# Performance work log

Measured on AMD Instinct MI355X. Metric: run time of the kernel, lower is better.

The kernel has to match this reference:

```python
import jax, jax.numpy as jnp
import numpy as np

B, C, H, W = 4, 768, 64, 64
NC_PRED = 200   # classes in preds/text (!= 171 to trigger retrieval path)
NC_MEM = 171    # memory/text_coco classes
TC = 256        # transform_channels
OC = 768        # out_channels
BN_EPS = 1e-5


def setup_inputs() -> dict:
    key = jax.random.key(0)
    ks = jax.random.split(key, 32)
    n = lambda k, s, sc=1.0: jax.random.normal(k, s, jnp.float32) * sc
    g = lambda k, c: 1.0 + 0.1 * jax.random.normal(k, (c,), jnp.float32)
    inp = {
        'feats': n(ks[0], (B, C, H, W)),
        'preds': n(ks[1], (B, NC_PRED, H, W)),
        'text': n(ks[2], (1, NC_PRED, 1, C)),
        'memory': n(ks[3], (NC_MEM, 1, C)),      # self.memory buffer
        'text_mem': n(ks[4], (NC_MEM, 1, C)),    # self.text buffer
        # query_project: two 1x1 conv + BN + ReLU
        'qw1': n(ks[5], (TC, C), C ** -0.5), 'qg1': g(ks[6], TC), 'qb1': n(ks[7], (TC,), 0.1),
        'qw2': n(ks[8], (TC, TC), TC ** -0.5), 'qg2': g(ks[9], TC), 'qb2': n(ks[10], (TC,), 0.1),
        # key_project: two 1x1 conv + BN + ReLU
        'kw1': n(ks[11], (TC, C), C ** -0.5), 'kg1': g(ks[12], TC), 'kb1': n(ks[13], (TC,), 0.1),
        'kw2': n(ks[14], (TC, TC), TC ** -0.5), 'kg2': g(ks[15], TC), 'kb2': n(ks[16], (TC,), 0.1),
        # value_project: 1x1 conv + BN + ReLU
        'vw': n(ks[17], (TC, C), C ** -0.5), 'vg': g(ks[18], TC), 'vb': n(ks[19], (TC,), 0.1),
        # out_project: 1x1 conv + BN + ReLU (TC -> C)
        'ow': n(ks[20], (C, TC), TC ** -0.5), 'og': g(ks[21], C), 'ob': n(ks[22], (C,), 0.1),
        # bottleneck: 3x3 conv (2C -> OC) + BN + ReLU
        'bw': n(ks[23], (OC, 2 * C, 3, 3), (2 * C * 9) ** -0.5), 'bg': g(ks[24], OC), 'bb': n(ks[25], (OC,), 0.1),
    }
    return inp


def _cbr(x, w, gamma, beta):
    # 1x1 conv (no bias) + eval-mode BN (mean=0, var=1) + ReLU
    y = jnp.einsum('oc,bchw->bohw', w, x)
    s = (gamma / jnp.sqrt(1.0 + BN_EPS))[None, :, None, None]
    return jax.nn.relu(y * s + beta[None, :, None, None])


def _forward(feats, preds, text, memory, text_mem,
             qw1, qg1, qb1, qw2, qg2, qb2,
             kw1, kg1, kb1, kw2, kg2, kb2,
             vw, vg, vb, ow, og, ob, bw, bg, bb):
    b, c, h, w = feats.shape
    nc = preds.shape[1]
    # softmax class weights per pixel: [B*H*W, NC]
    wcls = jax.nn.softmax(preds.transpose(0, 2, 3, 1).reshape(-1, nc), axis=-1)
    # --- retrieval: cosine sim + argmax + gather (nc != 171 branch) ---
    t = text[0, :, 0, :]          # [NC_PRED, C]
    tc = text_mem[:, 0, :]        # [NC_MEM, C]
    mem = memory[:, 0, :]         # [NC_MEM, C]
    den = jnp.linalg.norm(t, axis=1)[:, None] * jnp.linalg.norm(tc, axis=1)[None, :]
    sim = (t @ tc.T) / jnp.maximum(den, 1e-8)
    idx = jnp.argmax(sim, axis=1)            # [NC_PRED]
    D = mem[idx]                             # gathered memory rows [NC_PRED, C]
    # soft aggregation
    sel = (wcls @ D).reshape(b, h, w, c).transpose(0, 3, 1, 2)  # [B,C,H,W]
    # --- self-attention: query=feats, key/value=selected memory ---
    q = _cbr(_cbr(feats, qw1, qg1, qb1), qw2, qg2, qb2).reshape(b, TC, h * w).transpose(0, 2, 1)  # [B,HW,TC]
    k = _cbr(_cbr(sel, kw1, kg1, kb1), kw2, kg2, kb2).reshape(b, TC, h * w)                        # [B,TC,HW]
    v = _cbr(sel, vw, vg, vb).reshape(b, TC, h * w).transpose(0, 2, 1)                             # [B,HW,TC]
    att = jax.nn.softmax(jnp.einsum('bqc,bck->bqk', q, k) * (TC ** -0.5), axis=-1)                 # [B,HW,HW]
    ctx = jnp.einsum('bqk,bkc->bqc', att, v).transpose(0, 2, 1).reshape(b, TC, h, w)
    sel_out = _cbr(ctx, ow, og, ob)          # [B,C,H,W]
    # --- bottleneck: 3x3 conv + BN + ReLU on concat ---
    x = jnp.concatenate([feats, sel_out], axis=1)
    y = jax.lax.conv_general_dilated(x, bw, (1, 1), 'SAME',
                                     dimension_numbers=('NCHW', 'OIHW', 'NCHW'))
    s = (bg / jnp.sqrt(1.0 + BN_EPS))[None, :, None, None]
    return jax.nn.relu(y * s + bb[None, :, None, None])


def reference(feats, preds, text, memory, text_mem,
              qw1, qg1, qb1, qw2, qg2, qb2,
              kw1, kg1, kb1, kw2, kg2, kb2,
              vw, vg, vb, ow, og, ob, bw, bg, bb):
    return _forward(feats, preds, text, memory, text_mem,
                    qw1, qg1, qb1, qw2, qg2, qb2,
                    kw1, kg1, kb1, kw2, kg2, kb2,
                    vw, vg, vb, ow, og, ob, bw, bg, bb)
```

## Files before the change

kernel.cpp:

```cpp
#include <hip/hip_runtime.h>
#include <stdint.h>

typedef unsigned short u16;
typedef __attribute__((ext_vector_type(8))) short short8;
typedef __attribute__((ext_vector_type(4))) float f32x4;

#define RSQC 0.9999950000374997f
#define OUT_ELEMS 12582912

__device__ __forceinline__ float bf2f(u16 u) {
  union { uint32_t i; float f; } v; v.i = ((uint32_t)u) << 16; return v.f;
}
__device__ __forceinline__ u16 f2bf(float f) {
  union { uint32_t i; float f; } v; v.f = f;
  uint32_t i = v.i;
  i += 0x7fffu + ((i >> 16) & 1u);
  return (u16)(i >> 16);
}

__global__ __launch_bounds__(256) void probe_fill(float* out, float val) {
  for (size_t i = (size_t)blockIdx.x * 256 + threadIdx.x; i < OUT_ELEMS; i += (size_t)gridDim.x * 256)
    out[i] = val;
}


__global__ __launch_bounds__(64) void sim_argmax(const float* __restrict__ text,
                                                 const float* __restrict__ tmem,
                                                 int* __restrict__ idx) {
  const int i = blockIdx.x, lane = threadIdx.x;
  const float* t = text + (size_t)i * 768;
  float nt = 0.f;
  for (int c = lane; c < 768; c += 64) { float x = t[c]; nt += x * x; }
#pragma unroll
  for (int m = 32; m; m >>= 1) nt += __shfl_xor(nt, m);
  nt = sqrtf(nt);
  float best = -1e30f; int bj = 0x7fffffff;
  for (int j = lane; j < 171; j += 64) {
    const float* tc = tmem + (size_t)j * 768;
    float dot = 0.f, nc = 0.f;
    for (int c = 0; c < 768; ++c) {
      float y = tc[c];
      dot += t[c] * y;
      nc += y * y;
    }
    float den = fmaxf(nt * sqrtf(nc), 1e-8f);
    float s = dot / den;
    if (s > best || (s == best && j < bj)) { best = s; bj = j; }
  }
#pragma unroll
  for (int m = 32; m; m >>= 1) {
    float ob = __shfl_xor(best, m); int oj = __shfl_xor(bj, m);
    if (ob > best || (ob == best && oj < bj)) { best = ob; bj = oj; }
  }
  if (lane == 0) idx[i] = bj;
}

__global__ __launch_bounds__(256) void build_d(const float* __restrict__ memory,
                                               const int* __restrict__ idx,
                                               u16* __restrict__ D) {
  int i = blockIdx.x * 256 + threadIdx.x;
  if (i >= 256 * 768) return;
  int c = i % 768, j = i / 768;
  u16 v = 0;
  if (j < 200) {
    int ii = idx[j];
    ii = ii < 0 ? 0 : (ii > 170 ? 170 : ii);
    v = f2bf(memory[(size_t)ii * 768 + c]);
  }
  D[i] = v;
}

__global__ __launch_bounds__(256) void wcls_kernel(const float* __restrict__ preds,
                                                   u16* __restrict__ wcls) {
  __shared__ float red[4][64];
  const int tid = threadIdx.x;
  const int p = tid & 63, q = tid >> 6;
  const int pos = blockIdx.x * 64 + p;
  const int b = pos >> 12, hw = pos & 4095;
  const float* pp = preds + (size_t)b * 200 * 4096 + hw;
  const int nlo = q * 50, nhi = nlo + 50;
  float mx = -1e30f;
  for (int n = nlo; n < nhi; ++n) mx = fmaxf(mx, pp[(size_t)n * 4096]);
  red[q][p] = mx;
  __syncthreads();
  const float m = fmaxf(fmaxf(red[0][p], red[1][p]), fmaxf(red[2][p], red[3][p]));
  __syncthreads();
  float s = 0.f;
  for (int n = nlo; n < nhi; ++n) s += __expf(pp[(size_t)n * 4096] - m);
  red[q][p] = s;
  __syncthreads();
  const float inv = 1.f / (red[0][p] + red[1][p] + red[2][p] + red[3][p]);
  u16* w = wcls + (size_t)pos * 256;
#pragma unroll
  for (int c8 = 0; c8 < 8; ++c8) {
    short8 v;
    const int base = q * 64 + c8 * 8;
#pragma unroll
    for (int j = 0; j < 8; ++j) {
      const int n = base + j;
      float e = (n < 200) ? __expf(pp[(size_t)n * 4096] - m) * inv : 0.f;
      v[j] = (short)f2bf(e);
    }
    *(short8*)&w[base] = v;
  }
}

__global__ __launch_bounds__(256) void transpose_feats(const float* __restrict__ feats,
                                                       u16* __restrict__ ft) {
  __shared__ u16 t[64][65];
  const int bz = blockIdx.z, c0 = blockIdx.y * 64, p0 = blockIdx.x * 64;
  const int col = threadIdx.x & 63, row4 = threadIdx.x >> 6;
  const float* src = feats + ((size_t)bz * 768 + c0) * 4096 + p0;
#pragma unroll
  for (int i = 0; i < 16; ++i) {
    int ci = i * 4 + row4;
    t[ci][col] = f2bf(src[(size_t)ci * 4096 + col]);
  }
  __syncthreads();
  u16* dst = ft + ((size_t)bz * 4096 + p0) * 768 + c0;
#pragma unroll
  for (int i = 0; i < 16; ++i) {
    int pi = i * 4 + row4;
    dst[(size_t)pi * 768 + col] = t[col][pi];
  }
}

__global__ __launch_bounds__(256) void cast_all(
    const float* __restrict__ s0, u16* __restrict__ d0,
    const float* __restrict__ s1, u16* __restrict__ d1,
    const float* __restrict__ s2, u16* __restrict__ d2,
    const float* __restrict__ s3, u16* __restrict__ d3,
    const float* __restrict__ s4, u16* __restrict__ d4,
    const float* __restrict__ s5, u16* __restrict__ d5) {
  int i = blockIdx.x * 256 + threadIdx.x;
  if (i < 196608) d0[i] = f2bf(s0[i]);
  else if (i < 393216) d1[i - 196608] = f2bf(s1[i - 196608]);
  else if (i < 589824) d2[i - 393216] = f2bf(s2[i - 393216]);
  else if (i < 786432) d3[i - 589824] = f2bf(s3[i - 589824]);
  else if (i < 851968) d4[i - 786432] = f2bf(s4[i - 786432]);
  else if (i < 917504) d5[i - 851968] = f2bf(s5[i - 851968]);
}

__global__ __launch_bounds__(256) void repack_frag(const float* __restrict__ bw,
                                                   u16* __restrict__ w9f, int c_base) {
  size_t i = (size_t)blockIdx.x * 256 + threadIdx.x;
  if (i >= (size_t)5308416) return;
  int j = (int)(i & 7);
  int lane = (int)((i >> 3) & 63);
  int rem = (int)(i >> 9);
  int mfrag = rem % 48;
  int pt = rem / 48;
  int tap = pt % 9;
  int kc = pt / 9;
  int o = mfrag * 16 + (lane & 15);
  int c = kc * 32 + (lane >> 4) * 8 + j;
  w9f[i] = f2bf(bw[((size_t)o * 1536 + c_base + c) * 9 + tap]);
}


template <bool EP>
__global__ __launch_bounds__(256) void gemm_std(
    const u16* __restrict__ A, const u16* __restrict__ Bt, u16* __restrict__ out,
    const float* __restrict__ g, const float* __restrict__ bia,
    int N, int K, int lda, int ldb) {
  __shared__ __attribute__((aligned(16))) u16 As[2][128 * 32];
  __shared__ __attribute__((aligned(16))) u16 Bs[2][128 * 32];
  const int tid = threadIdx.x, lane = tid & 63, wv = tid >> 6;
  const int wr = wv >> 1, wc = wv & 1;
  const int m0 = blockIdx.y * 128, n0 = blockIdx.x * 128;
  const int r0 = lane >> 2, ksl = (lane & 3) * 8;
  const int wofs = (lane >> 2) * 32 + (((lane & 3) ^ ((lane >> 3) & 3)) << 3);
  const int rsl = (((lane >> 4) ^ ((lane >> 1) & 3)) << 3);
  f32x4 acc[4][4] = {};
  const int nt = K >> 5;

  short8 a0[2], b0[2], a1[2], b1[2];
  auto LOAD = [&](int t, short8 av[2], short8 bv[2]) {
    const int k0 = t << 5;
#pragma unroll
    for (int i = 0; i < 2; ++i) {
      const int row = (wv * 2 + i) * 16 + r0;
      av[i] = *(const short8*)(A + (size_t)(m0 + row) * lda + k0 + ksl);
      bv[i] = *(const short8*)(Bt + (size_t)(n0 + row) * ldb + k0 + ksl);
    }
  };
  auto STORE = [&](int buf, short8 av[2], short8 bv[2]) {
#pragma unroll
    for (int i = 0; i < 2; ++i) {
      const int o = (wv * 2 + i) * 512 + wofs;
      *(short8*)&As[buf][o] = av[i];
      *(short8*)&Bs[buf][o] = bv[i];
    }
  };
  auto COMPUTE = [&](int buf) {
    short8 a[4], b[4];
#pragma unroll
    for (int mi = 0; mi < 4; ++mi)
      a[mi] = *(const short8*)&As[buf][(wr * 4 + mi) * 512 + (lane & 15) * 32 + rsl];
#pragma unroll
    for (int ni = 0; ni < 4; ++ni)
      b[ni] = *(const short8*)&Bs[buf][(wc * 4 + ni) * 512 + (lane & 15) * 32 + rsl];
#pragma unroll
    for (int mi = 0; mi < 4; ++mi)
#pragma unroll
      for (int ni = 0; ni < 4; ++ni)
        acc[mi][ni] = __builtin_amdgcn_mfma_f32_16x16x32_bf16(a[mi], b[ni], acc[mi][ni], 0, 0, 0);
  };

  LOAD(0, a0, b0);
  for (int t = 0; t < nt; t += 2) {
    STORE(0, a0, b0);
    __syncthreads();
    LOAD(t + 1, a1, b1);
    COMPUTE(0);
    STORE(1, a1, b1);
    __syncthreads();
    if (t + 2 < nt) LOAD(t + 2, a0, b0);
    COMPUTE(1);
  }
  const int mb = m0 + wr * 64 + ((lane >> 4) << 2);
  const int nb = n0 + wc * 64 + (lane & 15);
#pragma unroll
  for (int ni = 0; ni < 4; ++ni) {
    const int n = nb + ni * 16;
    float s = 1.f, bb_ = 0.f;
    if (EP) { s = g[n] * RSQC; bb_ = bia[n]; }
#pragma unroll
    for (int mi = 0; mi < 4; ++mi)
#pragma unroll
      for (int r = 0; r < 4; ++r) {
        float v = acc[mi][ni][r];
        if (EP) v = fmaxf(v * s + bb_, 0.f);
        out[(size_t)(mb + mi * 16 + r) * N + n] = f2bf(v);
      }
  }
}

__global__ __launch_bounds__(256) void gemm_swv(
    const u16* __restrict__ A, const u16* __restrict__ Bt, u16* __restrict__ out,
    const float* __restrict__ g, const float* __restrict__ bia,
    int Mtot, int K, int lda, int ldb) {
  __shared__ __attribute__((aligned(16))) u16 As[2][128 * 32];
  __shared__ __attribute__((aligned(16))) u16 Bs[2][128 * 32];
  const int tid = threadIdx.x, lane = tid & 63, wv = tid >> 6;
  const int wr = wv >> 1, wc = wv & 1;
  const int m0 = blockIdx.y * 128, n0 = blockIdx.x * 128;
  const int r0 = lane >> 2, ksl = (lane & 3) * 8;
  const int wofs = (lane >> 2) * 32 + (((lane & 3) ^ ((lane >> 3) & 3)) << 3);
  const int rsl = (((lane >> 4) ^ ((lane >> 1) & 3)) << 3);
  f32x4 acc[4][4] = {};
  const int nt = K >> 5;

  short8 a0[2], b0[2], a1[2], b1[2];
  auto LOAD = [&](int t, short8 av[2], short8 bv[2]) {
    const int k0 = t << 5;
#pragma unroll
    for (int i = 0; i < 2; ++i) {
      const int row = (wv * 2 + i) * 16 + r0;
      av[i] = *(const short8*)(A + (size_t)(m0 + row) * lda + k0 + ksl);
      bv[i] = *(const short8*)(Bt + (size_t)(n0 + row) * ldb + k0 + ksl);
    }
  };
  auto STORE = [&](int buf, short8 av[2], short8 bv[2]) {
#pragma unroll
    for (int i = 0; i < 2; ++i) {
      const int o = (wv * 2 + i) * 512 + wofs;
      *(short8*)&As[buf][o] = av[i];
      *(short8*)&Bs[buf][o] = bv[i];
    }
  };
  auto COMPUTE = [&](int buf) {
    short8 a[4], b[4];
#pragma unroll
    for (int mi = 0; mi < 4; ++mi)
      a[mi] = *(const short8*)&As[buf][(wr * 4 + mi) * 512 + (lane & 15) * 32 + rsl];
#pragma unroll
    for (int ni = 0; ni < 4; ++ni)
      b[ni] = *(const short8*)&Bs[buf][(wc * 4 + ni) * 512 + (lane & 15) * 32 + rsl];
#pragma unroll
    for (int mi = 0; mi < 4; ++mi)
#pragma unroll
      for (int ni = 0; ni < 4; ++ni)
        acc[mi][ni] = __builtin_amdgcn_mfma_f32_16x16x32_bf16(a[mi], b[ni], acc[mi][ni], 0, 0, 0);
  };

  LOAD(0, a0, b0);
  for (int t = 0; t < nt; t += 2) {
    STORE(0, a0, b0);
    __syncthreads();
    LOAD(t + 1, a1, b1);
    COMPUTE(0);
    STORE(1, a1, b1);
    __syncthreads();
    if (t + 2 < nt) LOAD(t + 2, a0, b0);
    COMPUTE(1);
  }
  const int mb = m0 + wr * 64 + ((lane >> 4) << 2);
  const int nb = n0 + wc * 64 + (lane & 15);
#pragma unroll
  for (int mi = 0; mi < 4; ++mi)
#pragma unroll
    for (int r = 0; r < 4; ++r) {
      const int m = mb + mi * 16 + r;
      const float s = g[m] * RSQC, bb_ = bia[m];
#pragma unroll
      for (int ni = 0; ni < 4; ++ni) {
        const int n = nb + ni * 16;
        out[((size_t)(n >> 12) * Mtot + m) * 4096 + (n & 4095)] =
            f2bf(fmaxf(acc[mi][ni][r] * s + bb_, 0.f));
      }
    }
}

template <int MODE>
__global__ __launch_bounds__(256) void conv_frag(
    const u16* __restrict__ Af, const u16* __restrict__ X, float* out,
    const float* __restrict__ g, const float* __restrict__ bia) {
  __shared__ __attribute__((aligned(16))) u16 Hb[2][264 * 32];
  const int tid = threadIdx.x, lane = tid & 63, wv = tid >> 6;
  const int wr = wv >> 1, wc = wv & 1;
  const int id = blockIdx.y * 128 + blockIdx.x;
  const int xcd = id & 7, sl = id >> 3;
  const int m0 = (sl % 6) * 128;
  const int n0 = (xcd * 16 + sl / 6) * 128;
  f32x4 acc[4][4] = {};

  int vmask[4];
#pragma unroll
  for (int i = 0; i < 4; ++i) {
    const int hw = (n0 + wc * 64 + i * 16 + (lane & 15)) & 4095;
    const int h = hw >> 6, w = hw & 63;
    int m = 0;
#pragma unroll
    for (int t = 0; t < 9; ++t)
      if ((unsigned)(h + t / 3 - 1) < 64u && (unsigned)(w + t % 3 - 1) < 64u) m |= 1 << t;
    vmask[i] = m;
  }

  const int fb = (m0 >> 4) + wr * 4;
  auto aload = [&](int kc, int tap, short8 d[4]) {
    const u16* base = Af + ((size_t)((kc * 9 + tap) * 48 + fb) << 9) + lane * 8;
#pragma unroll
    for (int mi = 0; mi < 4; ++mi) d[mi] = *(const short8*)(base + (mi << 9));
  };
  auto hload = [&](int kc, short8 hreg[5]) {
#pragma unroll
    for (int j = 0; j < 5; ++j) {
      const int cid = tid + j * 256;
      if (cid < 1032) {
        int q = n0 - 65 + (cid >> 2);
        q = q < 0 ? 0 : (q > 16383 ? 16383 : q);
        hreg[j] = *(const short8*)(X + (size_t)q * 768 + kc * 32 + (cid & 3) * 8);
      }
    }
  };
  auto hwrite = [&](int buf, short8 hreg[5]) {
#pragma unroll
    for (int j = 0; j < 5; ++j) {
      const int cid = tid + j * 256;
      if (cid < 1032) {
        const int s = cid & 3, row = cid >> 2;
        *(short8*)((char*)&Hb[buf][0] + row * 64 + ((s ^ ((row >> 1) & 3)) << 4)) = hreg[j];
      }
    }
  };

  short8 hreg[5];
  hload(0, hreg);
  hwrite(0, hreg);
  __syncthreads();

  short8 acur[4], anxt[4];
  aload(0, 0, acur);
  int p = 0;
  for (int kc = 0; kc < 24; ++kc) {
    if (kc < 23) hload(kc + 1, hreg);
#pragma unroll
    for (int tap = 0; tap < 9; ++tap) {
      const int nk = (tap == 8) ? (kc == 23 ? 23 : kc + 1) : kc;
      const int ntp = (tap == 8) ? 0 : tap + 1;
      aload(nk, ntp, anxt);
      const int shift = (tap / 3 - 1) * 64 + (tap % 3 - 1);
#pragma unroll
      for (int ni = 0; ni < 4; ++ni) {
        const int hrow = wc * 64 + ni * 16 + (lane & 15) + 65 + shift;
        short8 bv = *(const short8*)((const char*)&Hb[p][0] + hrow * 64 +
                                     (((lane >> 4) ^ ((hrow >> 1) & 3)) << 4));
        short8 z = {};
        if (!((vmask[ni] >> tap) & 1)) bv = z;
#pragma unroll
        for (int mi = 0; mi < 4; ++mi)
          acc[mi][ni] = __builtin_amdgcn_mfma_f32_16x16x32_bf16(acur[mi], bv, acc[mi][ni], 0, 0, 0);
      }
#pragma unroll
      for (int mi = 0; mi < 4; ++mi) acur[mi] = anxt[mi];
    }
    if (kc < 23) {
      hwrite(p ^ 1, hreg);
      __syncthreads();
      p ^= 1;
    }
  }
  const int mb = m0 + wr * 64 + ((lane >> 4) << 2);
  const int nb = n0 + wc * 64 + (lane & 15);
#pragma unroll
  for (int mi = 0; mi < 4; ++mi)
#pragma unroll
    for (int r = 0; r < 4; ++r) {
      const int m = mb + mi * 16 + r;
      float s = 0.f, bb_ = 0.f;
      if (MODE == 2) { s = g[m] * RSQC; bb_ = bia[m]; }
#pragma unroll
      for (int ni = 0; ni < 4; ++ni) {
        const int n = nb + ni * 16;
        const size_t oidx = ((size_t)(n >> 12) * 768 + m) * 4096 + (n & 4095);
        if (MODE == 1) out[oidx] = acc[mi][ni][r];
        else out[oidx] = fmaxf((acc[mi][ni][r] + out[oidx]) * s + bb_, 0.f);
      }
    }
}

__global__ __launch_bounds__(256) void flash_attn(const u16* Q,
                                                  const u16* __restrict__ Kg,
                                                  const u16* __restrict__ Vt,
                                                  u16* ctx) {
  __shared__ __attribute__((aligned(16))) u16 KVs[64 * 256];
  __shared__ __attribute__((aligned(16))) u16 Ps[4096];
  const int tid = threadIdx.x, lane = tid & 63, wv = tid >> 6;
  const int b = blockIdx.y, q0 = blockIdx.x * 64;
  const u16* qb = Q + ((size_t)b * 4096 + q0) * 256;
  const u16* kb = Kg + (size_t)b * 4096 * 256;
  const u16* vb = Vt + (size_t)b * 256 * 4096;
  const float scale = 0.0625f;

  short8 qf[8];
  {
    const int arow = wv * 16 + (lane & 15);
    const u16* qrow = qb + (size_t)arow * 256 + (lane >> 4) * 8;
#pragma unroll
    for (int kk = 0; kk < 8; ++kk) qf[kk] = *(const short8*)(qrow + kk * 32);
  }
  float mreg[4] = {-1e30f, -1e30f, -1e30f, -1e30f};
  float lsum[4] = {0.f, 0.f, 0.f, 0.f};
  f32x4 o[16] = {};

  for (int t = 0; t < 64; ++t) {
    {
      const int r = tid >> 5, sb = (tid & 31) * 16;
      const char* ksrc = (const char*)(kb + (size_t)t * 64 * 256);
#pragma unroll
      for (int i = 0; i < 8; ++i) {
        int row = i * 8 + r;
        short8 v = *(const short8*)(ksrc + (size_t)row * 512 + sb);
        *(short8*)((char*)KVs + row * 512 + (sb ^ ((row & 7) << 4))) = v;
      }
    }
    __syncthreads();
    f32x4 s4[4] = {};
    __builtin_amdgcn_s_setprio(1);
#pragma unroll
    for (int kk = 0; kk < 8; ++kk) {
      const int cb = (kk * 32 + ((lane >> 4) * 8)) * 2;
#pragma unroll
      for (int ni = 0; ni < 4; ++ni) {
        const int brow = ni * 16 + (lane & 15);
        short8 bb = *(const short8*)((const char*)KVs + brow * 512 + (cb ^ ((brow & 7) << 4)));
        s4[ni] = __builtin_amdgcn_mfma_f32_16x16x32_bf16(qf[kk], bb, s4[ni], 0, 0, 0);
      }
    }
    __builtin_amdgcn_s_setprio(0);
    float al[4], p[4][4];
#pragma unroll
    for (int r = 0; r < 4; ++r) {
      float v0 = fmaxf(fmaxf(s4[0][r], s4[1][r]), fmaxf(s4[2][r], s4[3][r]));
      v0 = fmaxf(v0, __shfl_xor(v0, 1));
      v0 = fmaxf(v0, __shfl_xor(v0, 2));
      v0 = fmaxf(v0, __shfl_xor(v0, 4));
      v0 = fmaxf(v0, __shfl_xor(v0, 8));
      const float mn = fmaxf(mreg[r], v0 * scale);
      al[r] = __expf(mreg[r] - mn);
      mreg[r] = mn;
      float srow = 0.f;
#pragma unroll
      for (int ni = 0; ni < 4; ++ni) {
        float pv = __expf(s4[ni][r] * scale - mn);
        p[ni][r] = pv;
        srow += pv;
      }
      srow += __shfl_xor(srow, 1);
      srow += __shfl_xor(srow, 2);
      srow += __shfl_xor(srow, 4);
      srow += __shfl_xor(srow, 8);
      lsum[r] = lsum[r] * al[r] + srow;
    }
#pragma unroll
    for (int nf = 0; nf < 16; ++nf)
#pragma unroll
      for (int r = 0; r < 4; ++r) o[nf][r] *= al[r];
    {
      char* pbase = (char*)Ps + wv * 2048;
#pragma unroll
      for (int ni = 0; ni < 4; ++ni)
#pragma unroll
        for (int r = 0; r < 4; ++r) {
          const int row = ((lane >> 4) << 2) + r, col = ni * 16 + (lane & 15);
          *(u16*)(pbase + row * 128 + ((col * 2) ^ ((row & 7) << 4))) = f2bf(p[ni][r]);
        }
    }
    __syncthreads();
    {
      const int slot = tid & 7;
#pragma unroll
      for (int i = 0; i < 8; ++i) {
        const int cc = i * 32 + (tid >> 3);
        short8 v = *(const short8*)((const char*)vb + ((size_t)cc * 4096 + t * 64) * 2 + slot * 16);
        *(short8*)((char*)KVs + cc * 128 + ((slot * 16) ^ ((cc & 7) << 4))) = v;
      }
    }
    __syncthreads();
    short8 pa[2];
#pragma unroll
    for (int kk = 0; kk < 2; ++kk) {
      const int row = lane & 15;
      const int cb = (kk * 32 + ((lane >> 4) * 8)) * 2;
      pa[kk] = *(const short8*)((const char*)Ps + wv * 2048 + row * 128 + (cb ^ ((row & 7) << 4)));
    }
    __builtin_amdgcn_s_setprio(1);
#pragma unroll
    for (int nf = 0; nf < 16; ++nf) {
      const int crow = nf * 16 + (lane & 15);
#pragma unroll
      for (int kk = 0; kk < 2; ++kk) {
        const int kb2 = (kk * 32 + ((lane >> 4) * 8)) * 2;
        short8 bb = *(const short8*)((const char*)KVs + crow * 128 + (kb2 ^ ((crow & 7) << 4)));
        o[nf] = __builtin_amdgcn_mfma_f32_16x16x32_bf16(pa[kk], bb, o[nf], 0, 0, 0);
      }
    }
    __builtin_amdgcn_s_setprio(0);
    __syncthreads();
  }
  u16* cb_ = ctx + ((size_t)b * 4096 + q0) * 256;
#pragma unroll
  for (int r = 0; r < 4; ++r) {
    const int row = wv * 16 + ((lane >> 4) << 2) + r;
    const float inv = 1.f / lsum[r];
#pragma unroll
    for (int nf = 0; nf < 16; ++nf) {
      const int col = nf * 16 + (lane & 15);
      cb_[(size_t)row * 256 + col] = f2bf(o[nf][r] * inv);
    }
  }
}


extern "C" void kernel_launch(void* const* d_in, const int* in_sizes, int n_in,
                              void* d_out, int out_size, void* d_ws, size_t ws_size,
                              hipStream_t stream) {
  (void)in_sizes; (void)n_in; (void)out_size;
  const float* feats  = (const float*)d_in[0];
  const float* preds  = (const float*)d_in[1];
  const float* text   = (const float*)d_in[2];
  const float* memory = (const float*)d_in[3];
  const float* tmem   = (const float*)d_in[4];
  const float* qw1 = (const float*)d_in[5];  const float* qg1 = (const float*)d_in[6];  const float* qb1 = (const float*)d_in[7];
  const float* qw2 = (const float*)d_in[8];  const float* qg2 = (const float*)d_in[9];  const float* qb2 = (const float*)d_in[10];
  const float* kw1 = (const float*)d_in[11]; const float* kg1 = (const float*)d_in[12]; const float* kb1 = (const float*)d_in[13];
  const float* kw2 = (const float*)d_in[14]; const float* kg2 = (const float*)d_in[15]; const float* kb2 = (const float*)d_in[16];
  const float* vw  = (const float*)d_in[17]; const float* vg  = (const float*)d_in[18]; const float* vb  = (const float*)d_in[19];
  const float* ow  = (const float*)d_in[20]; const float* og  = (const float*)d_in[21]; const float* ob  = (const float*)d_in[22];
  const float* bw  = (const float*)d_in[23]; const float* bg  = (const float*)d_in[24]; const float* bb  = (const float*)d_in[25];

  float* dout = (float*)d_out;
  char* ws = (char*)d_ws;
  u16* featsT = (u16*)(ws);
  u16* selout = (u16*)(ws + 25165824);
  u16* S2     = (u16*)(ws + 50331648);
  u16* qw1c   = (u16*)(ws + 58720256);
  u16* kw1c   = (u16*)(ws + 59113472);
  u16* vwc    = (u16*)(ws + 59506688);
  u16* owc    = (u16*)(ws + 59899904);
  u16* qw2c   = (u16*)(ws + 60293120);
  u16* kw2c   = (u16*)(ws + 60424192);
  u16* w9     = S2;
  const size_t WS_NEED = 60948480;
  u16* D   = selout;
  u16* KD  = (u16*)((char*)selout + 393216);
  u16* VD  = (u16*)((char*)selout + 524288);
  int* idx = (int*)((char*)selout + 655360);
  u16* O0 = (u16*)dout;
  u16* O1 = O0 + 4194304;
  u16* O2 = O0 + 8388608;

  if (ws_size < WS_NEED) {
    probe_fill<<<2048, 256, 0, stream>>>(dout, 1000.0f);
    return;
  }

  u16* wcls = O0;
  u16* k1 = S2, *q1 = S2;
  u16* kbuf = O1, *vT = O2;
  u16* qbuf = O0, *ctx = O0;

  sim_argmax<<<200, 64, 0, stream>>>(text, tmem, idx);
  build_d<<<768, 256, 0, stream>>>(memory, idx, D);
  wcls_kernel<<<256, 256, 0, stream>>>(preds, wcls);
  transpose_feats<<<dim3(64, 12, 4), 256, 0, stream>>>(feats, featsT);
  cast_all<<<3584, 256, 0, stream>>>(qw1, qw1c, kw1, kw1c, vw, vwc, ow, owc, qw2, qw2c, kw2, kw2c);

  gemm_std<false><<<dim3(2, 2), 256, 0, stream>>>(kw1c, D, KD, nullptr, nullptr, 256, 768, 768, 768);
  gemm_std<false><<<dim3(2, 2), 256, 0, stream>>>(vwc, D, VD, nullptr, nullptr, 256, 768, 768, 768);

  gemm_std<true><<<dim3(2, 128), 256, 0, stream>>>(wcls, KD, k1, kg1, kb1, 256, 256, 256, 256);
  gemm_std<true><<<dim3(2, 128), 256, 0, stream>>>(k1, kw2c, kbuf, kg2, kb2, 256, 256, 256, 256);
  gemm_swv<<<dim3(128, 2), 256, 0, stream>>>(VD, wcls, vT, vg, vb, 256, 256, 256, 256);
  gemm_std<true><<<dim3(2, 128), 256, 0, stream>>>(featsT, qw1c, q1, qg1, qb1, 256, 768, 768, 768);
  gemm_std<true><<<dim3(2, 128), 256, 0, stream>>>(q1, qw2c, qbuf, qg2, qb2, 256, 256, 256, 256);
  flash_attn<<<dim3(64, 4), 256, 0, stream>>>(qbuf, kbuf, vT, ctx);
  gemm_std<true><<<dim3(6, 128), 256, 0, stream>>>(ctx, owc, selout, og, ob, 768, 256, 256, 256);
  repack_frag<<<20736, 256, 0, stream>>>(bw, w9, 0);
  conv_frag<1><<<dim3(128, 6), 256, 0, stream>>>(w9, featsT, dout, nullptr, nullptr);
  repack_frag<<<20736, 256, 0, stream>>>(bw, w9, 768);
  conv_frag<2><<<dim3(128, 6), 256, 0, stream>>>(w9, selout, dout, bg, bb);
}
```

Baseline: 815.4 us.

## Vectorize weight repack and stage conv halo via direct global-to-LDS loads

```diff
diff --git a/kernel.cpp b/kernel.cpp
--- a/kernel.cpp
+++ b/kernel.cpp
@@ -16,6 +16,11 @@
   uint32_t i = v.i;
   i += 0x7fffu + ((i >> 16) & 1u);
   return (u16)(i >> 16);
+}
+__device__ __forceinline__ void gload16(const u16* g, u16* l) {
+  __builtin_amdgcn_global_load_lds(
+      (const __attribute__((address_space(1))) uint32_t*)g,
+      (__attribute__((address_space(3))) uint32_t*)l, 16, 0, 0);
 }
 
 __global__ __launch_bounds__(256) void probe_fill(float* out, float val) {
@@ -141,22 +146,25 @@
   else if (i < 917504) d5[i - 851968] = f2bf(s5[i - 851968]);
 }
 
-__global__ __launch_bounds__(256) void repack_frag(const float* __restrict__ bw,
-                                                   u16* __restrict__ w9f, int c_base) {
-  size_t i = (size_t)blockIdx.x * 256 + threadIdx.x;
-  if (i >= (size_t)5308416) return;
-  int j = (int)(i & 7);
-  int lane = (int)((i >> 3) & 63);
-  int rem = (int)(i >> 9);
-  int mfrag = rem % 48;
-  int pt = rem / 48;
-  int tap = pt % 9;
-  int kc = pt / 9;
-  int o = mfrag * 16 + (lane & 15);
-  int c = kc * 32 + (lane >> 4) * 8 + j;
-  w9f[i] = f2bf(bw[((size_t)o * 1536 + c_base + c) * 9 + tap]);
-}
-
+__global__ __launch_bounds__(256) void repack2(const float* __restrict__ bw,
+                                               u16* __restrict__ w9f, int c_base) {
+  const int gid = blockIdx.x * 4 + (threadIdx.x >> 6);
+  const int lane = threadIdx.x & 63;
+  const int mfrag = gid % 48, kc = gid / 48;
+  const int o = mfrag * 16 + (lane & 15);
+  const int c = c_base + kc * 32 + (lane >> 4) * 8;
+  const float* src = bw + ((size_t)o * 1536 + c) * 9;
+  float v[72];
+#pragma unroll
+  for (int t = 0; t < 72; ++t) v[t] = src[t];
+#pragma unroll
+  for (int tap = 0; tap < 9; ++tap) {
+    short8 w;
+#pragma unroll
+    for (int j = 0; j < 8; ++j) w[j] = (short)f2bf(v[j * 9 + tap]);
+    *(short8*)&w9f[(((size_t)(kc * 9 + tap) * 48 + mfrag) << 9) + lane * 8] = w;
+  }
+}
 
 template <bool EP>
 __global__ __launch_bounds__(256) void gemm_std(
@@ -343,43 +351,38 @@
 #pragma unroll
     for (int mi = 0; mi < 4; ++mi) d[mi] = *(const short8*)(base + (mi << 9));
   };
-  auto hload = [&](int kc, short8 hreg[5]) {
+  auto hstage = [&](int kc, int buf) {
 #pragma unroll
     for (int j = 0; j < 5; ++j) {
       const int cid = tid + j * 256;
       if (cid < 1032) {
         int q = n0 - 65 + (cid >> 2);
         q = q < 0 ? 0 : (q > 16383 ? 16383 : q);
-        hreg[j] = *(const short8*)(X + (size_t)q * 768 + kc * 32 + (cid & 3) * 8);
-      }
-    }
-  };
-  auto hwrite = [&](int buf, short8 hreg[5]) {
-#pragma unroll
-    for (int j = 0; j < 5; ++j) {
-      const int cid = tid + j * 256;
-      if (cid < 1032) {
-        const int s = cid & 3, row = cid >> 2;
-        *(short8*)((char*)&Hb[buf][0] + row * 64 + ((s ^ ((row >> 1) & 3)) << 4)) = hreg[j];
-      }
-    }
-  };
-
-  short8 hreg[5];
-  hload(0, hreg);
-  hwrite(0, hreg);
+        const int row = cid >> 2;
+        const int s = (cid & 3) ^ ((row >> 1) & 3);
+        gload16(X + (size_t)q * 768 + kc * 32 + s * 8, &Hb[buf][(size_t)cid * 8]);
+      }
+    }
+  };
+
+  short8 ab0[4], ab1[4], ab2[4];
+  hstage(0, 0);
+  aload(0, 0, ab0);
+  aload(0, 1, ab1);
   __syncthreads();
-
-  short8 acur[4], anxt[4];
-  aload(0, 0, acur);
   int p = 0;
   for (int kc = 0; kc < 24; ++kc) {
-    if (kc < 23) hload(kc + 1, hreg);
+    if (kc < 23) hstage(kc + 1, p ^ 1);
 #pragma unroll
     for (int tap = 0; tap < 9; ++tap) {
-      const int nk = (tap == 8) ? (kc == 23 ? 23 : kc + 1) : kc;
-      const int ntp = (tap == 8) ? 0 : tap + 1;
-      aload(nk, ntp, anxt);
+      {
+        int ft = tap + 2, fkc = kc;
+        if (ft >= 9) { ft -= 9; ++fkc; }
+        if (fkc > 23) { fkc = 23; }
+        short8* dst = (tap % 3 == 0) ? ab2 : (tap % 3 == 1) ? ab0 : ab1;
+        aload(fkc, ft, dst);
+      }
+      const short8* cur = (tap % 3 == 0) ? ab0 : (tap % 3 == 1) ? ab1 : ab2;
       const int shift = (tap / 3 - 1) * 64 + (tap % 3 - 1);
 #pragma unroll
       for (int ni = 0; ni < 4; ++ni) {
@@ -390,16 +393,11 @@
         if (!((vmask[ni] >> tap) & 1)) bv = z;
 #pragma unroll
         for (int mi = 0; mi < 4; ++mi)
-          acc[mi][ni] = __builtin_amdgcn_mfma_f32_16x16x32_bf16(acur[mi], bv, acc[mi][ni], 0, 0, 0);
-      }
-#pragma unroll
-      for (int mi = 0; mi < 4; ++mi) acur[mi] = anxt[mi];
-    }
-    if (kc < 23) {
-      hwrite(p ^ 1, hreg);
-      __syncthreads();
-      p ^= 1;
-    }
+          acc[mi][ni] = __builtin_amdgcn_mfma_f32_16x16x32_bf16(cur[mi], bv, acc[mi][ni], 0, 0, 0);
+      }
+    }
+    __syncthreads();
+    if (kc < 23) p ^= 1;
   }
   const int mb = m0 + wr * 64 + ((lane >> 4) << 2);
   const int nb = n0 + wc * 64 + (lane & 15);
@@ -617,8 +615,8 @@
   gemm_std<true><<<dim3(2, 128), 256, 0, stream>>>(q1, qw2c, qbuf, qg2, qb2, 256, 256, 256, 256);
   flash_attn<<<dim3(64, 4), 256, 0, stream>>>(qbuf, kbuf, vT, ctx);
   gemm_std<true><<<dim3(6, 128), 256, 0, stream>>>(ctx, owc, selout, og, ob, 768, 256, 256, 256);
-  repack_frag<<<20736, 256, 0, stream>>>(bw, w9, 0);
+  repack2<<<288, 256, 0, stream>>>(bw, w9, 0);
   conv_frag<1><<<dim3(128, 6), 256, 0, stream>>>(w9, featsT, dout, nullptr, nullptr);
-  repack_frag<<<20736, 256, 0, stream>>>(bw, w9, 768);
+  repack2<<<288, 256, 0, stream>>>(bw, w9, 768);
   conv_frag<2><<<dim3(128, 6), 256, 0, stream>>>(w9, selout, dout, bg, bb);
 }
```

Measured after the change: 857.1 us. 5.1% more time.
